# Kernel tuning notes

Measured on AMD Instinct MI355X. Metric: run time of the kernel, lower is better.

## Reference

```python
import jax, jax.numpy as jnp
import numpy as np

INF = jnp.float32(1e9)


def _nearest_zero_dist_axis0(is_zero):
    """1D distance (in index units) to the nearest True along axis 0.

    is_zero: bool array [L, ...]. Returns float32 [L, ...].
    """
    d0 = jnp.where(is_zero, jnp.float32(0.0), INF)

    def step(c, d):
        c = jnp.minimum(c + 1.0, d)
        return c, c

    init = jnp.full(d0.shape[1:], INF, dtype=jnp.float32)
    _, fwd = jax.lax.scan(step, init, d0)
    _, bwd = jax.lax.scan(step, init, d0[::-1])
    return jnp.minimum(fwd, bwd[::-1])


def _minplus_parabola_axis0(g2):
    """Exact squared-EDT lower envelope along axis 0.

    g2: float32 [L, ...] of squared distances. Returns
    out[i, ...] = min_k ( (i-k)^2 + g2[k, ...] ).
    Brute-force min-plus, scanned over output index to bound memory.
    """
    L = g2.shape[0]
    k = jnp.arange(L, dtype=jnp.float32)

    def step(_, i):
        # (i - k)^2 broadcast against all source positions k
        par = (i - k) ** 2  # [L]
        par = par.reshape((L,) + (1,) * (g2.ndim - 1))
        return None, jnp.min(par + g2, axis=0)  # [...]

    _, out = jax.lax.scan(step, None, jnp.arange(L, dtype=jnp.float32))
    return out  # [L, ...]


def _edt(x):
    """Exact N-D Euclidean distance transform matching scipy's
    distance_transform_edt: distance from each nonzero element to the
    nearest zero element, over all dims of x."""
    is_zero = (x == 0)
    # Pass 1 (axis 0): exact 1D distance to nearest zero along axis 0.
    d = _nearest_zero_dist_axis0(is_zero)  # [B,H,W]
    d2 = d * d
    # Passes 2..n: exact min-plus with squared parabola along each
    # remaining axis, applied to the running squared distance field.
    for ax in range(1, x.ndim):
        d2 = jnp.moveaxis(d2, ax, 0)
        d2 = _minplus_parabola_axis0(d2)
        d2 = jnp.moveaxis(d2, 0, ax)
    return jnp.sqrt(d2)


def setup_inputs() -> dict:
    key = jax.random.key(0)
    B, H, W = 16, 512, 512
    x = (jax.random.uniform(key, (B, H, W)) > 0.05).astype(jnp.float32)
    return {"x": x}


def reference(x) -> jnp.ndarray:
    distance = _edt(x)
    # distance[x.isnan()] = nan  (NaN inputs are nonzero -> foreground,
    # then their output is masked to NaN, as in the torch module)
    return jnp.where(jnp.isnan(x), jnp.nan, distance)
```

## Files before the change

### kernel.cpp

```cpp
#include <hip/hip_runtime.h>
#include <math.h>
#include <stdint.h>

#define NB 16
#define NH 512
#define NW 512
#define PLANE (NH * NW)
#define INF_D 1.0e9f
#define INF2 1.0e18f
#define BIG 3.0e38f
#define NSEG 64
#define TWB 8
#define HROW 516

__device__ __forceinline__ void eval_minplus(const float* __restrict__ hrow,
                                             const float* __restrict__ sminw,
                                             int q, float* best,
                                             const float* neg2i,
                                             const float* ifl) {
    float bmax = BIG;
    for (int step = 0; step < 2 * NSEG - 1; ++step) {
        int r = (step + 1) >> 1;
        float gapf = (float)(8 * (r - 1) + 1);
        float gap2 = gapf * gapf;
        if ((step & 1) && gap2 >= bmax) break;
        int s = (step & 1) ? (q - r) : (q + r);
        if (s < 0 || s >= NSEG) continue;
        if (step && (gap2 + sminw[s * TWB] >= bmax)) continue;
        const float* hp = hrow + s * 8;
        float4 A = *reinterpret_cast<const float4*>(hp);
        float4 B = *reinterpret_cast<const float4*>(hp + 4);
        float s8f = (float)(s * 8);
#pragma unroll
        for (int j = 0; j < 8; ++j) {
            float n2 = neg2i[j];
            float c0 = fmaf(n2, s8f, A.x);
            float c1 = fmaf(n2, s8f + 1.0f, A.y);
            float c2 = fmaf(n2, s8f + 2.0f, A.z);
            float c3 = fmaf(n2, s8f + 3.0f, A.w);
            float c4 = fmaf(n2, s8f + 4.0f, B.x);
            float c5 = fmaf(n2, s8f + 5.0f, B.y);
            float c6 = fmaf(n2, s8f + 6.0f, B.z);
            float c7 = fmaf(n2, s8f + 7.0f, B.w);
            float bb = fminf(fminf(best[j], c0), c1);
            bb = fminf(fminf(bb, c2), c3);
            bb = fminf(fminf(bb, c4), c5);
            bb = fminf(fminf(bb, c6), c7);
            best[j] = bb;
        }
        float t0 = fmaf(ifl[0], ifl[0], best[0]);
        float t1 = fmaf(ifl[1], ifl[1], best[1]);
        float t2 = fmaf(ifl[2], ifl[2], best[2]);
        float t3 = fmaf(ifl[3], ifl[3], best[3]);
        float t4 = fmaf(ifl[4], ifl[4], best[4]);
        float t5 = fmaf(ifl[5], ifl[5], best[5]);
        float t6 = fmaf(ifl[6], ifl[6], best[6]);
        float t7 = fmaf(ifl[7], ifl[7], best[7]);
        float m = fmaxf(fmaxf(t0, t1), t2);
        m = fmaxf(fmaxf(m, t3), t4);
        m = fmaxf(fmaxf(m, t5), t6);
        bmax = fmaxf(m, t7);
    }
}

__global__ __launch_bounds__(256, 4) void k_pass_b(const float* __restrict__ x,
                                                   unsigned char* __restrict__ code) {
    int col = blockIdx.x * 256 + threadIdx.x;
    float d0[NB], dd[NB];
    int nanb = 0;
#pragma unroll
    for (int b = 0; b < NB; ++b) {
        float v = x[(size_t)b * PLANE + col];
        nanb |= (isnan(v) ? (1 << b) : 0);
        d0[b] = (v == 0.0f) ? 0.0f : INF_D;
    }
    float cc = INF_D;
#pragma unroll
    for (int b = 0; b < NB; ++b) { cc = fminf(cc + 1.0f, d0[b]); dd[b] = cc; }
    cc = INF_D;
#pragma unroll
    for (int b = NB - 1; b >= 0; --b) { cc = fminf(cc + 1.0f, d0[b]); dd[b] = fminf(dd[b], cc); }
#pragma unroll
    for (int b = 0; b < NB; ++b) {
        int di = (dd[b] >= 1.0e8f) ? 31 : (int)dd[b];
        code[(size_t)b * PLANE + col] =
            (unsigned char)(di | (((nanb >> b) & 1) << 7));
    }
}

__global__ __launch_bounds__(512, 4) void k_pass_h(const unsigned char* __restrict__ code,
                                                   float* __restrict__ out) {
    __shared__ float hs[TWB * HROW];
    __shared__ float smin[NSEG * TWB];
    __shared__ unsigned int flgw[NH * 2];
    int t = threadIdx.x;
    int b = blockIdx.y;
    int w0 = blockIdx.x * TWB;
    const unsigned char* gb8 = code + (size_t)b * PLANE + w0;

    for (int m = t; m < 1024; m += 512) {
        int k = m >> 1;
        int bo = (m & 1) * 4;
        unsigned int u = *reinterpret_cast<const unsigned int*>(gb8 + (size_t)k * NW + bo);
        int kk = k * k;
#pragma unroll
        for (int e = 0; e < 4; ++e) {
            int c = (u >> (8 * e)) & 0xFF;
            int dl = c & 31;
            hs[(bo + e) * HROW + k] = (dl == 31) ? INF2 : (float)(dl * dl + kk);
        }
        flgw[m] = (u >> 7) & 0x01010101u;
    }
    __syncthreads();
    {
        int s = t >> 3, w = t & 7;
        const float* hp = &hs[w * HROW + s * 8];
        float4 A = *reinterpret_cast<const float4*>(hp);
        float4 B = *reinterpret_cast<const float4*>(hp + 4);
        int k0 = s * 8;
        float m0 = fminf(fminf(A.x - (float)(k0 * k0), A.y - (float)((k0 + 1) * (k0 + 1))),
                         A.z - (float)((k0 + 2) * (k0 + 2)));
        float m1 = fminf(fminf(A.w - (float)((k0 + 3) * (k0 + 3)), B.x - (float)((k0 + 4) * (k0 + 4))),
                         B.y - (float)((k0 + 5) * (k0 + 5)));
        float m2 = fminf(B.z - (float)((k0 + 6) * (k0 + 6)), B.w - (float)((k0 + 7) * (k0 + 7)));
        smin[t] = fminf(fminf(m0, m1), m2);
    }
    __syncthreads();

    int w = t & 7, q = t >> 3;
    int i0 = q * 8;
    float best[8], neg2i[8], ifl[8];
#pragma unroll
    for (int j = 0; j < 8; ++j) {
        best[j] = BIG;
        ifl[j] = (float)(i0 + j);
        neg2i[j] = (float)(-2 * (i0 + j));
    }
    eval_minplus(&hs[w * HROW], &smin[w], q, best, neg2i, ifl);

    const unsigned char* flgb = reinterpret_cast<const unsigned char*>(flgw);
    float wgf = (float)(w0 + w);
    float* ob = out + (size_t)b * PLANE + w0 + w;
#pragma unroll
    for (int j = 0; j < 8; ++j) {
        float v = fmaf(ifl[j], ifl[j], best[j]);
        float v2 = fmaf(wgf, wgf, v);
        unsigned int bits = __float_as_uint(v2) |
                            ((unsigned int)flgb[(i0 + j) * TWB + w] << 31);
        ob[(size_t)(i0 + j) * NW] = __uint_as_float(bits);
    }
}

__global__ __launch_bounds__(512, 4) void k_pass_w(float* __restrict__ out) {
    __shared__ float hs[TWB * HROW];
    __shared__ float smin[NSEG * TWB];
    __shared__ unsigned int flgw[NH * 2];
    int t = threadIdx.x;
    int line0 = blockIdx.x * TWB;
    float* gb = out + (size_t)line0 * NW;

    for (int m = t; m < 1024; m += 512) {
        float4 v = *reinterpret_cast<const float4*>(gb + (size_t)m * 4);
        int line = m >> 7;
        int k = (m * 4) & 511;
        unsigned int u0 = __float_as_uint(v.x), u1 = __float_as_uint(v.y);
        unsigned int u2 = __float_as_uint(v.z), u3 = __float_as_uint(v.w);
        flgw[m] = (u0 >> 31) | ((u1 >> 31) << 8) |
                  ((u2 >> 31) << 16) | ((u3 >> 31) << 24);
        float4 o;
        o.x = __uint_as_float(u0 & 0x7fffffffu);
        o.y = __uint_as_float(u1 & 0x7fffffffu);
        o.z = __uint_as_float(u2 & 0x7fffffffu);
        o.w = __uint_as_float(u3 & 0x7fffffffu);
        *reinterpret_cast<float4*>(&hs[line * HROW + k]) = o;
    }
    __syncthreads();
    {
        int s = t >> 3, line = t & 7;
        const float* hp = &hs[line * HROW + s * 8];
        float4 A = *reinterpret_cast<const float4*>(hp);
        float4 B = *reinterpret_cast<const float4*>(hp + 4);
        int k0 = s * 8;
        float m0 = fminf(fminf(A.x - (float)(k0 * k0), A.y - (float)((k0 + 1) * (k0 + 1))),
                         A.z - (float)((k0 + 2) * (k0 + 2)));
        float m1 = fminf(fminf(A.w - (float)((k0 + 3) * (k0 + 3)), B.x - (float)((k0 + 4) * (k0 + 4))),
                         B.y - (float)((k0 + 5) * (k0 + 5)));
        float m2 = fminf(B.z - (float)((k0 + 6) * (k0 + 6)), B.w - (float)((k0 + 7) * (k0 + 7)));
        smin[t] = fminf(fminf(m0, m1), m2);
    }
    __syncthreads();

    int line = t & 7, q = t >> 3;
    int i0 = q * 8;
    float best[8], neg2i[8], ifl[8];
#pragma unroll
    for (int j = 0; j < 8; ++j) {
        best[j] = BIG;
        ifl[j] = (float)(i0 + j);
        neg2i[j] = (float)(-2 * (i0 + j));
    }
    eval_minplus(&hs[line * HROW], &smin[line], q, best, neg2i, ifl);

    unsigned int f0 = flgw[(line * NW + i0) >> 2];
    unsigned int f1 = flgw[((line * NW + i0) >> 2) + 1];
    float v[8];
#pragma unroll
    for (int j = 0; j < 8; ++j) {
        float m = fmaf(ifl[j], ifl[j], best[j]);
        float sq = sqrtf(m);
        unsigned int fb = (j < 4) ? ((f0 >> (8 * j)) & 1u)
                                  : ((f1 >> (8 * (j - 4))) & 1u);
        v[j] = fb ? __builtin_nanf("") : sq;
    }
    float* op = gb + (size_t)line * NW + i0;
    float4 oa, ob4;
    oa.x = v[0]; oa.y = v[1]; oa.z = v[2]; oa.w = v[3];
    ob4.x = v[4]; ob4.y = v[5]; ob4.z = v[6]; ob4.w = v[7];
    *reinterpret_cast<float4*>(op) = oa;
    *reinterpret_cast<float4*>(op + 4) = ob4;
}

extern "C" void kernel_launch(void* const* d_in, const int* in_sizes, int n_in,
                              void* d_out, int out_size, void* d_ws, size_t ws_size,
                              hipStream_t stream) {
    (void)in_sizes; (void)n_in; (void)out_size; (void)ws_size;
    const float* x = (const float*)d_in[0];
    float* out = (float*)d_out;
    unsigned char* code = (unsigned char*)d_ws;

    k_pass_b<<<dim3(PLANE / 256), 256, 0, stream>>>(x, code);
    k_pass_h<<<dim3(NW / TWB, NB), 512, 0, stream>>>(code, out);
    k_pass_w<<<dim3(NB * NH / TWB), 512, 0, stream>>>(out);
}
```

Before: 36.89 us.

## Replace adaptive outward segment search with fixed neighbor pass plus radius-bounded window

The min-plus envelope search no longer walks outward segment by segment with per-step pruning from a shared-memory table of per-segment minima. It first evaluates the three nearest segments, takes the resulting worst-case squared distance as a search radius, and then scans every segment inside that radius. This removes the smin precompute pass and one __syncthreads per kernel, and makes the loop control uniform. In exchange it can evaluate segments the old lower-bound test would have skipped, and wide radii (e.g. INF rows) trigger full scans.

```diff
diff --git a/kernel.cpp b/kernel.cpp
--- a/kernel.cpp
+++ b/kernel.cpp
@@ -13,53 +13,62 @@
 #define TWB 8
 #define HROW 516
 
+__device__ __forceinline__ void eval_seg(const float* __restrict__ hrow,
+                                         int ss, float* best,
+                                         const float* neg2i) {
+    const float* hp = hrow + ss * 8;
+    float4 A = *reinterpret_cast<const float4*>(hp);
+    float4 B = *reinterpret_cast<const float4*>(hp + 4);
+    float s8f = (float)(ss * 8);
+#pragma unroll
+    for (int j = 0; j < 8; ++j) {
+        float n2 = neg2i[j];
+        float c0 = fmaf(n2, s8f, A.x);
+        float c1 = fmaf(n2, s8f + 1.0f, A.y);
+        float c2 = fmaf(n2, s8f + 2.0f, A.z);
+        float c3 = fmaf(n2, s8f + 3.0f, A.w);
+        float c4 = fmaf(n2, s8f + 4.0f, B.x);
+        float c5 = fmaf(n2, s8f + 5.0f, B.y);
+        float c6 = fmaf(n2, s8f + 6.0f, B.z);
+        float c7 = fmaf(n2, s8f + 7.0f, B.w);
+        float bb = fminf(fminf(best[j], c0), c1);
+        bb = fminf(fminf(bb, c2), c3);
+        bb = fminf(fminf(bb, c4), c5);
+        bb = fminf(fminf(bb, c6), c7);
+        best[j] = bb;
+    }
+}
+
 __device__ __forceinline__ void eval_minplus(const float* __restrict__ hrow,
-                                             const float* __restrict__ sminw,
                                              int q, float* best,
                                              const float* neg2i,
                                              const float* ifl) {
-    float bmax = BIG;
-    for (int step = 0; step < 2 * NSEG - 1; ++step) {
-        int r = (step + 1) >> 1;
-        float gapf = (float)(8 * (r - 1) + 1);
-        float gap2 = gapf * gapf;
-        if ((step & 1) && gap2 >= bmax) break;
-        int s = (step & 1) ? (q - r) : (q + r);
-        if (s < 0 || s >= NSEG) continue;
-        if (step && (gap2 + sminw[s * TWB] >= bmax)) continue;
-        const float* hp = hrow + s * 8;
-        float4 A = *reinterpret_cast<const float4*>(hp);
-        float4 B = *reinterpret_cast<const float4*>(hp + 4);
-        float s8f = (float)(s * 8);
-#pragma unroll
-        for (int j = 0; j < 8; ++j) {
-            float n2 = neg2i[j];
-            float c0 = fmaf(n2, s8f, A.x);
-            float c1 = fmaf(n2, s8f + 1.0f, A.y);
-            float c2 = fmaf(n2, s8f + 2.0f, A.z);
-            float c3 = fmaf(n2, s8f + 3.0f, A.w);
-            float c4 = fmaf(n2, s8f + 4.0f, B.x);
-            float c5 = fmaf(n2, s8f + 5.0f, B.y);
-            float c6 = fmaf(n2, s8f + 6.0f, B.z);
-            float c7 = fmaf(n2, s8f + 7.0f, B.w);
-            float bb = fminf(fminf(best[j], c0), c1);
-            bb = fminf(fminf(bb, c2), c3);
-            bb = fminf(fminf(bb, c4), c5);
-            bb = fminf(fminf(bb, c6), c7);
-            best[j] = bb;
-        }
-        float t0 = fmaf(ifl[0], ifl[0], best[0]);
-        float t1 = fmaf(ifl[1], ifl[1], best[1]);
-        float t2 = fmaf(ifl[2], ifl[2], best[2]);
-        float t3 = fmaf(ifl[3], ifl[3], best[3]);
-        float t4 = fmaf(ifl[4], ifl[4], best[4]);
-        float t5 = fmaf(ifl[5], ifl[5], best[5]);
-        float t6 = fmaf(ifl[6], ifl[6], best[6]);
-        float t7 = fmaf(ifl[7], ifl[7], best[7]);
-        float m = fmaxf(fmaxf(t0, t1), t2);
-        m = fmaxf(fmaxf(m, t3), t4);
-        m = fmaxf(fmaxf(m, t5), t6);
-        bmax = fmaxf(m, t7);
+    int s_lo0 = (q > 0) ? q - 1 : 0;
+    int s_hi0 = (q < NSEG - 1) ? q + 1 : NSEG - 1;
+    for (int ss = s_lo0; ss <= s_hi0; ++ss) eval_seg(hrow, ss, best, neg2i);
+
+    float t0 = fmaf(ifl[0], ifl[0], best[0]);
+    float t1 = fmaf(ifl[1], ifl[1], best[1]);
+    float t2 = fmaf(ifl[2], ifl[2], best[2]);
+    float t3 = fmaf(ifl[3], ifl[3], best[3]);
+    float t4 = fmaf(ifl[4], ifl[4], best[4]);
+    float t5 = fmaf(ifl[5], ifl[5], best[5]);
+    float t6 = fmaf(ifl[6], ifl[6], best[6]);
+    float t7 = fmaf(ifl[7], ifl[7], best[7]);
+    float m = fmaxf(fmaxf(t0, t1), t2);
+    m = fmaxf(fmaxf(m, t3), t4);
+    m = fmaxf(fmaxf(m, t5), t6);
+    float bmax = fmaxf(m, t7);
+
+    int sw = (int)sqrtf(bmax) + 1;
+    int i0 = q * 8;
+    int s_lo = (i0 - sw) >> 3;
+    int s_hi = (i0 + 7 + sw) >> 3;
+    if (s_lo < 0) s_lo = 0;
+    if (s_hi > NSEG - 1) s_hi = NSEG - 1;
+    for (int ss = s_lo; ss <= s_hi; ++ss) {
+        if (ss >= s_lo0 && ss <= s_hi0) continue;
+        eval_seg(hrow, ss, best, neg2i);
     }
 }
 
@@ -91,7 +100,6 @@
 __global__ __launch_bounds__(512, 4) void k_pass_h(const unsigned char* __restrict__ code,
                                                    float* __restrict__ out) {
     __shared__ float hs[TWB * HROW];
-    __shared__ float smin[NSEG * TWB];
     __shared__ unsigned int flgw[NH * 2];
     int t = threadIdx.x;
     int b = blockIdx.y;
@@ -112,20 +120,6 @@
         flgw[m] = (u >> 7) & 0x01010101u;
     }
     __syncthreads();
-    {
-        int s = t >> 3, w = t & 7;
-        const float* hp = &hs[w * HROW + s * 8];
-        float4 A = *reinterpret_cast<const float4*>(hp);
-        float4 B = *reinterpret_cast<const float4*>(hp + 4);
-        int k0 = s * 8;
-        float m0 = fminf(fminf(A.x - (float)(k0 * k0), A.y - (float)((k0 + 1) * (k0 + 1))),
-                         A.z - (float)((k0 + 2) * (k0 + 2)));
-        float m1 = fminf(fminf(A.w - (float)((k0 + 3) * (k0 + 3)), B.x - (float)((k0 + 4) * (k0 + 4))),
-                         B.y - (float)((k0 + 5) * (k0 + 5)));
-        float m2 = fminf(B.z - (float)((k0 + 6) * (k0 + 6)), B.w - (float)((k0 + 7) * (k0 + 7)));
-        smin[t] = fminf(fminf(m0, m1), m2);
-    }
-    __syncthreads();
 
     int w = t & 7, q = t >> 3;
     int i0 = q * 8;
@@ -136,7 +130,7 @@
         ifl[j] = (float)(i0 + j);
         neg2i[j] = (float)(-2 * (i0 + j));
     }
-    eval_minplus(&hs[w * HROW], &smin[w], q, best, neg2i, ifl);
+    eval_minplus(&hs[w * HROW], q, best, neg2i, ifl);
 
     const unsigned char* flgb = reinterpret_cast<const unsigned char*>(flgw);
     float wgf = (float)(w0 + w);
@@ -153,7 +147,6 @@
 
 __global__ __launch_bounds__(512, 4) void k_pass_w(float* __restrict__ out) {
     __shared__ float hs[TWB * HROW];
-    __shared__ float smin[NSEG * TWB];
     __shared__ unsigned int flgw[NH * 2];
     int t = threadIdx.x;
     int line0 = blockIdx.x * TWB;
@@ -175,20 +168,6 @@
         *reinterpret_cast<float4*>(&hs[line * HROW + k]) = o;
     }
     __syncthreads();
-    {
-        int s = t >> 3, line = t & 7;
-        const float* hp = &hs[line * HROW + s * 8];
-        float4 A = *reinterpret_cast<const float4*>(hp);
-        float4 B = *reinterpret_cast<const float4*>(hp + 4);
-        int k0 = s * 8;
-        float m0 = fminf(fminf(A.x - (float)(k0 * k0), A.y - (float)((k0 + 1) * (k0 + 1))),
-                         A.z - (float)((k0 + 2) * (k0 + 2)));
-        float m1 = fminf(fminf(A.w - (float)((k0 + 3) * (k0 + 3)), B.x - (float)((k0 + 4) * (k0 + 4))),
-                         B.y - (float)((k0 + 5) * (k0 + 5)));
-        float m2 = fminf(B.z - (float)((k0 + 6) * (k0 + 6)), B.w - (float)((k0 + 7) * (k0 + 7)));
-        smin[t] = fminf(fminf(m0, m1), m2);
-    }
-    __syncthreads();
 
     int line = t & 7, q = t >> 3;
     int i0 = q * 8;
@@ -199,7 +178,7 @@
         ifl[j] = (float)(i0 + j);
         neg2i[j] = (float)(-2 * (i0 + j));
     }
-    eval_minplus(&hs[line * HROW], &smin[line], q, best, neg2i, ifl);
+    eval_minplus(&hs[line * HROW], q, best, neg2i, ifl);
 
     unsigned int f0 = flgw[(line * NW + i0) >> 2];
     unsigned int f1 = flgw[((line * NW + i0) >> 2) + 1];
```

New measurement: 36.51 us (median of 2 runs). Within noise of the previous version (-1.0%).
